# Kernel optimization log

Hardware: AMD Instinct MI355X
Metric: run time of the kernel (lower is better)

## Reference

```python
import jax, jax.numpy as jnp
import numpy as np

VOC, DIM = 50000, 128
B, CTX, K = 256, 8, 10


def setup_inputs() -> dict:
    key = jax.random.key(0)
    k1, k2, k3, k4, k5 = jax.random.split(key, 5)
    # one-hot inputs, as the module's math assumes (one-hot matmul == gather)
    vo_idx = jax.random.randint(k1, (B,), 0, VOC)
    vi_idx = jax.random.randint(k2, (B, CTX), 0, VOC)
    neg_idx = jax.random.randint(k3, (B, K), 0, VOC)
    vo = jax.nn.one_hot(vo_idx, VOC, dtype=jnp.float32)            # [B, VOC]
    vi = jax.nn.one_hot(vi_idx, VOC, dtype=jnp.float32)           # [B, CTX, VOC]
    neg_samples = jax.nn.one_hot(neg_idx, VOC, dtype=jnp.float32) # [B, K, VOC]
    V = jax.random.normal(k4, (VOC, DIM), dtype=jnp.float32)
    U = jax.random.normal(k5, (VOC, DIM), dtype=jnp.float32)
    return {"vo": vo, "vi": vi, "neg_samples": neg_samples, "V": V, "U": U}


def reference(vo, vi, neg_samples, V, U):
    vo_embed = vo @ V                                           # [B, D]
    # matmul(vi, U).mean(dim=1): fold mean into a single contraction
    vi_embed = jnp.einsum('bcv,vd->bd', vi, U) / vi.shape[1]    # [B, D]
    left = jax.nn.log_sigmoid(jnp.sum(vo_embed * vi_embed, axis=1, keepdims=True))  # [B,1]
    neg_embed = jnp.einsum('bkv,vd->bkd', neg_samples, U)       # [B, K, D]
    batch_mul = jnp.einsum('bkd,bd->bk', neg_embed, vo_embed)   # [B, K]
    right = jnp.sum(jax.nn.log_sigmoid(-batch_mul), axis=1, keepdims=True)          # [B,1]
    return jnp.mean(-(left + right))
```

## Files before the change

kernel.cpp:

```cpp
#include <hip/hip_runtime.h>
#include <hip/hip_bf16.h>
#include <math.h>

#define VOC 50000
#define DIM 128
#define B   256
#define CTX 8
#define K   10

#define NVEC (VOC / 4)
#define N_VO  (B)
#define N_VI  (B * CTX)
#define N_NEG (B * K)
#define NROW  (N_VO + N_VI + N_NEG)

__global__ __launch_bounds__(256) void find_indices(
    const float* __restrict__ vo,
    const float* __restrict__ vi,
    const float* __restrict__ neg,
    int* __restrict__ out_idx)
{
    const int r = blockIdx.x;
    const float* row;
    if (r < N_VO)              row = vo  + (size_t)r * VOC;
    else if (r < N_VO + N_VI)  row = vi  + (size_t)(r - N_VO) * VOC;
    else                       row = neg + (size_t)(r - N_VO - N_VI) * VOC;

    const float4* row4 = (const float4*)row;

    __shared__ int found;
    if (threadIdx.x == 0) found = -1;
    __syncthreads();

    for (int start = 0; start < NVEC; start += 256 * 4) {
#pragma unroll
        for (int j = 0; j < 4; ++j) {
            const int p = start + j * 256 + (int)threadIdx.x;
            if (p < NVEC) {
                const float4 v = row4[p];
                if (v.x != 0.f || v.y != 0.f || v.z != 0.f || v.w != 0.f) {
                    int lane_off = (v.x != 0.f) ? 0 : (v.y != 0.f) ? 1
                                 : (v.z != 0.f) ? 2 : 3;
                    found = 4 * p + lane_off;
                }
            }
        }
        __syncthreads();
        if (found >= 0) break;
    }

    if (threadIdx.x == 0) out_idx[r] = found;
}

__device__ __forceinline__ float wave_sum(float v) {
#pragma unroll
    for (int o = 32; o > 0; o >>= 1) v += __shfl_down(v, o);
    return v;
}

__device__ __forceinline__ float log_sigmoid(float x) {
    return fminf(x, 0.f) - log1pf(expf(-fabsf(x)));
}

__global__ __launch_bounds__(64) void cbow_loss(
    const float* __restrict__ V,
    const float* __restrict__ U,
    const int* __restrict__ idx_all,
    float* __restrict__ out)
{
    const int b = blockIdx.x;
    const int t = threadIdx.x;

    const int* idx_vo  = idx_all;
    const int* idx_vi  = idx_all + N_VO;
    const int* idx_neg = idx_all + N_VO + N_VI;

    const int vo_i = max(idx_vo[b], 0);
    const float v0 = V[(size_t)vo_i * DIM + t];
    const float v1 = V[(size_t)vo_i * DIM + t + 64];

    float e0 = 0.f, e1 = 0.f;
#pragma unroll
    for (int c = 0; c < CTX; ++c) {
        const int u = max(idx_vi[b * CTX + c], 0);
        e0 += U[(size_t)u * DIM + t];
        e1 += U[(size_t)u * DIM + t + 64];
    }
    e0 *= (1.f / CTX);
    e1 *= (1.f / CTX);

    const float dot_pos = wave_sum(v0 * e0 + v1 * e1);

    float right = 0.f;
#pragma unroll
    for (int k = 0; k < K; ++k) {
        const int u = max(idx_neg[b * K + k], 0);
        const float s = wave_sum(v0 * U[(size_t)u * DIM + t] +
                                 v1 * U[(size_t)u * DIM + t + 64]);
        if (t == 0) right += log_sigmoid(-s);
    }

    if (t == 0) {
        const float left = log_sigmoid(dot_pos);
        atomicAdd(out, -(left + right) * (1.f / B));
    }
}

extern "C" void kernel_launch(void* const* d_in, const int* in_sizes, int n_in,
                              void* d_out, int out_size, void* d_ws, size_t ws_size,
                              hipStream_t stream) {
    const float* vo  = (const float*)d_in[0];
    const float* vi  = (const float*)d_in[1];
    const float* neg = (const float*)d_in[2];
    const float* V   = (const float*)d_in[3];
    const float* U   = (const float*)d_in[4];
    float* out = (float*)d_out;

    int* idx_ws = (int*)d_ws;

    hipMemsetAsync(out, 0, sizeof(float), stream);

    find_indices<<<NROW, 256, 0, stream>>>(vo, vi, neg, idx_ws);
    cbow_loss<<<B, 64, 0, stream>>>(V, U, idx_ws, out);
}
```

Baseline: 870.4 us.

## Scan one-hot rows per wavefront with ballot early exit and nontemporal loads

The index-finding kernel now assigns one 64-lane wavefront per one-hot row, four rows per block. Each wave finds the first nonzero with a ballot and exits on its own, which removes the shared-memory flag and the block-wide barriers. Loads are issued as nontemporal vector loads, aiming for more memory parallelism and shorter scans. The loss kernel switches to float2 loads and clamps indices on both ends. The risk is a stale index in the workspace: a row with no nonzero never writes its slot, where the old kernel wrote -1.

```diff
diff --git a/kernel.cpp b/kernel.cpp
--- a/kernel.cpp
+++ b/kernel.cpp
@@ -1,5 +1,4 @@
 #include <hip/hip_runtime.h>
-#include <hip/hip_bf16.h>
 #include <math.h>
 
 #define VOC 50000
@@ -14,42 +13,54 @@
 #define N_NEG (B * K)
 #define NROW  (N_VO + N_VI + N_NEG)
 
+#define ROWS_PER_BLOCK 4
+
+typedef float f32x4 __attribute__((ext_vector_type(4)));
+
 __global__ __launch_bounds__(256) void find_indices(
     const float* __restrict__ vo,
     const float* __restrict__ vi,
     const float* __restrict__ neg,
     int* __restrict__ out_idx)
 {
-    const int r = blockIdx.x;
+    const int wave = threadIdx.x >> 6;
+    const int lane = threadIdx.x & 63;
+    const int r = blockIdx.x * ROWS_PER_BLOCK + wave;
+
     const float* row;
     if (r < N_VO)              row = vo  + (size_t)r * VOC;
     else if (r < N_VO + N_VI)  row = vi  + (size_t)(r - N_VO) * VOC;
     else                       row = neg + (size_t)(r - N_VO - N_VI) * VOC;
 
-    const float4* row4 = (const float4*)row;
+    const f32x4* row4 = (const f32x4*)row;
 
-    __shared__ int found;
-    if (threadIdx.x == 0) found = -1;
-    __syncthreads();
-
-    for (int start = 0; start < NVEC; start += 256 * 4) {
+    for (int s = 0; s < NVEC; s += 4 * 64) {
+        f32x4 v[4];
 #pragma unroll
         for (int j = 0; j < 4; ++j) {
-            const int p = start + j * 256 + (int)threadIdx.x;
-            if (p < NVEC) {
-                const float4 v = row4[p];
-                if (v.x != 0.f || v.y != 0.f || v.z != 0.f || v.w != 0.f) {
-                    int lane_off = (v.x != 0.f) ? 0 : (v.y != 0.f) ? 1
-                                 : (v.z != 0.f) ? 2 : 3;
-                    found = 4 * p + lane_off;
-                }
+            int p = s + j * 64 + lane;
+            p = (p < NVEC) ? p : (NVEC - 1);
+            v[j] = __builtin_nontemporal_load(&row4[p]);
+        }
+        int found_j = -1;
+#pragma unroll
+        for (int j = 3; j >= 0; --j) {
+            if (v[j].x != 0.f || v[j].y != 0.f || v[j].z != 0.f || v[j].w != 0.f)
+                found_j = j;
+        }
+        const unsigned long long m = __ballot(found_j >= 0);
+        if (m != 0ull) {
+            if (lane == __ffsll(m) - 1) {
+                int p = s + found_j * 64 + lane;
+                p = (p < NVEC) ? p : (NVEC - 1);
+                const f32x4 u = v[found_j];
+                const int off = (u.x != 0.f) ? 0 : (u.y != 0.f) ? 1
+                              : (u.z != 0.f) ? 2 : 3;
+                out_idx[r] = 4 * p + off;
             }
+            break;
         }
-        __syncthreads();
-        if (found >= 0) break;
     }
-
-    if (threadIdx.x == 0) out_idx[r] = found;
 }
 
 __device__ __forceinline__ float wave_sum(float v) {
@@ -60,6 +71,10 @@
 
 __device__ __forceinline__ float log_sigmoid(float x) {
     return fminf(x, 0.f) - log1pf(expf(-fabsf(x)));
+}
+
+__device__ __forceinline__ int clamp_idx(int i) {
+    return i < 0 ? 0 : (i >= VOC ? VOC - 1 : i);
 }
 
 __global__ __launch_bounds__(64) void cbow_loss(
@@ -75,28 +90,28 @@
     const int* idx_vi  = idx_all + N_VO;
     const int* idx_neg = idx_all + N_VO + N_VI;
 
-    const int vo_i = max(idx_vo[b], 0);
-    const float v0 = V[(size_t)vo_i * DIM + t];
-    const float v1 = V[(size_t)vo_i * DIM + t + 64];
+    const int vo_i = clamp_idx(idx_vo[b]);
+    const float2 v = ((const float2*)(V + (size_t)vo_i * DIM))[t];
 
-    float e0 = 0.f, e1 = 0.f;
+    float2 e = make_float2(0.f, 0.f);
 #pragma unroll
     for (int c = 0; c < CTX; ++c) {
-        const int u = max(idx_vi[b * CTX + c], 0);
-        e0 += U[(size_t)u * DIM + t];
-        e1 += U[(size_t)u * DIM + t + 64];
+        const int u = clamp_idx(idx_vi[b * CTX + c]);
+        const float2 uu = ((const float2*)(U + (size_t)u * DIM))[t];
+        e.x += uu.x;
+        e.y += uu.y;
     }
-    e0 *= (1.f / CTX);
-    e1 *= (1.f / CTX);
+    e.x *= (1.f / CTX);
+    e.y *= (1.f / CTX);
 
-    const float dot_pos = wave_sum(v0 * e0 + v1 * e1);
+    const float dot_pos = wave_sum(v.x * e.x + v.y * e.y);
 
     float right = 0.f;
 #pragma unroll
     for (int k = 0; k < K; ++k) {
-        const int u = max(idx_neg[b * K + k], 0);
-        const float s = wave_sum(v0 * U[(size_t)u * DIM + t] +
-                                 v1 * U[(size_t)u * DIM + t + 64]);
+        const int u = clamp_idx(idx_neg[b * K + k]);
+        const float2 uu = ((const float2*)(U + (size_t)u * DIM))[t];
+        const float s = wave_sum(v.x * uu.x + v.y * uu.y);
         if (t == 0) right += log_sigmoid(-s);
     }
 
@@ -120,6 +135,6 @@
 
     hipMemsetAsync(out, 0, sizeof(float), stream);
 
-    find_indices<<<NROW, 256, 0, stream>>>(vo, vi, neg, idx_ws);
+    find_indices<<<NROW / ROWS_PER_BLOCK, 256, 0, stream>>>(vo, vi, neg, idx_ws);
     cbow_loss<<<B, 64, 0, stream>>>(V, U, idx_ws, out);
 }
```

Result: faster. 827.2 us (-5.0%).
